# Kernel optimization log

Hardware: AMD Instinct MI355X
Metric: run time of the kernel (lower is better)

Reference implementation:

```python
import jax, jax.numpy as jnp
import numpy as np

# ---- config (mirrors module init_kwargs) ----
PRE_NMS_TOP_N = 4096
POST_NMS_TOP_N = 300
NMS_THRESH = 0.5
MIN_SIZE = 0
IMG_H = 640
IMG_W = 640
BBOX_XFORM_CLIP = float(np.log(1000.0 / 16.0))  # exp clamp in BoxCoder.decode
NEG = -1e9  # score sentinel for suppressed boxes
TO_REMOVE = 1.0


def setup_inputs() -> dict:
    key = jax.random.key(0)
    k1, k2, k3 = jax.random.split(key, 3)
    N, A, H, W, C = 16, 3, 160, 160, 80
    objectness = jax.random.normal(k1, (N, A, H, W), jnp.float32)
    box_regression = jax.random.normal(k2, (N, A * 4, H, W), jnp.float32) * 0.5
    cls = jax.random.normal(k3, (N, A * C, H, W), jnp.float32)
    # grid anchors in xyxy, ordering matches permute_and_flatten (H, W, A)
    stride = IMG_W / W
    xs = (np.arange(W, dtype=np.float32) + 0.5) * stride
    ys = (np.arange(H, dtype=np.float32) + 0.5) * stride
    cy, cx = np.meshgrid(ys, xs, indexing="ij")  # [H,W]
    half = np.array([32.0, 64.0, 128.0], dtype=np.float32) / 2.0  # A anchor sizes
    x1 = cx[..., None] - half
    y1 = cy[..., None] - half
    x2 = cx[..., None] + half - 1.0
    y2 = cy[..., None] + half - 1.0
    anch = np.stack([x1, y1, x2, y2], axis=-1).reshape(-1, 4).astype(np.float32)
    anchors = jnp.broadcast_to(jnp.asarray(anch), (N,) + anch.shape)  # [N, A*H*W, 4]
    return {"anchors": anchors, "objectness": objectness,
            "box_regression": box_regression, "cls": cls}


def _permute_and_flatten(x, N, A, C, H, W):
    # (N, A*C, H, W) -> (N, H*W*A, C)
    return x.reshape(N, A, C, H, W).transpose(0, 3, 4, 1, 2).reshape(N, H * W * A, C)


def _decode(rel, anc):
    # BoxCoder(weights=(1,1,1,1)).decode ; rel, anc: [..., 4] xyxy anchors
    w = anc[..., 2] - anc[..., 0] + TO_REMOVE
    h = anc[..., 3] - anc[..., 1] + TO_REMOVE
    cx = anc[..., 0] + 0.5 * w
    cy = anc[..., 1] + 0.5 * h
    dx, dy = rel[..., 0], rel[..., 1]
    dw = jnp.minimum(rel[..., 2], BBOX_XFORM_CLIP)
    dh = jnp.minimum(rel[..., 3], BBOX_XFORM_CLIP)
    pcx = dx * w + cx
    pcy = dy * h + cy
    pw = jnp.exp(dw) * w
    ph = jnp.exp(dh) * h
    return jnp.stack([pcx - 0.5 * pw, pcy - 0.5 * ph,
                      pcx + 0.5 * pw - 1.0, pcy + 0.5 * ph - 1.0], axis=-1)


def _iou_one_vs_all(b, boxes):
    area_b = (b[2] - b[0] + TO_REMOVE) * (b[3] - b[1] + TO_REMOVE)
    areas = (boxes[:, 2] - boxes[:, 0] + TO_REMOVE) * (boxes[:, 3] - boxes[:, 1] + TO_REMOVE)
    iw = jnp.clip(jnp.minimum(b[2], boxes[:, 2]) - jnp.maximum(b[0], boxes[:, 0]) + TO_REMOVE, 0.0)
    ih = jnp.clip(jnp.minimum(b[3], boxes[:, 3]) - jnp.maximum(b[1], boxes[:, 1]) + TO_REMOVE, 0.0)
    inter = iw * ih
    return inter / (area_b + areas - inter)


def _nms_indices(boxes, scores):
    # greedy NMS, fixed POST_NMS_TOP_N iterations; returns (idx[K], valid[K])
    K = POST_NMS_TOP_N

    def body(i, state):
        sc, idx, val = state
        j = jnp.argmax(sc)
        s = sc[j]
        iou = _iou_one_vs_all(boxes[j], boxes)
        sc = jnp.where(iou > NMS_THRESH, NEG, sc).at[j].set(NEG)
        return sc, idx.at[i].set(j.astype(jnp.int32)), val.at[i].set(s > NEG / 2)

    idx0 = jnp.zeros((K,), jnp.int32)
    val0 = jnp.zeros((K,), bool)
    _, idx, val = jax.lax.fori_loop(0, K, body, (scores, idx0, val0))
    return idx, val


def _forward(anchors, objectness, box_regression, cls):
    N, A, H, W = objectness.shape
    C = cls.shape[1] // A
    obj = jax.nn.sigmoid(_permute_and_flatten(objectness, N, A, 1, H, W).reshape(N, -1))
    cls_f = _permute_and_flatten(cls, N, A, C, H, W)          # [N, P, C]
    reg = _permute_and_flatten(box_regression, N, A, 4, H, W)  # [N, P, 4]

    k1 = min(PRE_NMS_TOP_N, A * H * W)
    scores, topk_idx = jax.lax.top_k(obj, k1)                  # [N, K1]
    b = jnp.arange(N)[:, None]
    reg_t = reg[b, topk_idx]                                   # [N, K1, 4]
    cls_t = cls_f[b, topk_idx]                                 # [N, K1, C]
    anch_t = anchors[b, topk_idx]                              # [N, K1, 4]

    proposals = _decode(reg_t, anch_t)                         # [N, K1, 4]
    labels = jnp.argmax(cls_t, axis=-1) + 1                    # [N, K1]

    # clip_to_image(remove_empty=False)
    x1 = jnp.clip(proposals[..., 0], 0.0, IMG_W - TO_REMOVE)
    y1 = jnp.clip(proposals[..., 1], 0.0, IMG_H - TO_REMOVE)
    x2 = jnp.clip(proposals[..., 2], 0.0, IMG_W - TO_REMOVE)
    y2 = jnp.clip(proposals[..., 3], 0.0, IMG_H - TO_REMOVE)
    boxes = jnp.stack([x1, y1, x2, y2], axis=-1)

    # remove_small_boxes: keep via score masking (keeps shapes static)
    keep = ((x2 - x1 + TO_REMOVE) >= MIN_SIZE) & ((y2 - y1 + TO_REMOVE) >= MIN_SIZE)
    masked_scores = jnp.where(keep, scores, NEG)

    nms_idx, nms_valid = jax.vmap(_nms_indices)(
        jax.lax.stop_gradient(boxes), jax.lax.stop_gradient(masked_scores))

    sel_boxes = boxes[b, nms_idx]                              # [N, K2, 4]
    sel_scores = scores[b, nms_idx]                            # [N, K2]
    sel_labels = labels[b, nms_idx].astype(jnp.float32)

    sel_boxes = jnp.where(nms_valid[..., None], sel_boxes, 0.0)
    sel_scores = jnp.where(nms_valid, sel_scores, 0.0)
    sel_labels = jnp.where(nms_valid, sel_labels, 0.0)
    # [N, K2, 6] = boxes(4) | score(1) | label(1)
    return jnp.concatenate([sel_boxes, sel_scores[..., None], sel_labels[..., None]], axis=-1)


def reference(anchors, objectness, box_regression, cls):
    return _forward(anchors, objectness, box_regression, cls)
```

## Files before the change

kernel.cpp:

```cpp
#include <hip/hip_runtime.h>
#include <math.h>

#define NIMG 16
#define A_ 3
#define H_ 160
#define W_ 160
#define C_ 80
#define HW_ (H_*W_)
#define P_ (HW_*A_)
#define K1 4096
#define K2 300
#define CAND_CAP 8192
#define IMGMAX 639.0f
#define BBOX_CLIP 4.135166556742356f
#define IOU_THR (0.5 + 1.0/67108864.0)

#define RING_ROWS 128
#define GRP 16
#define NGRP (K1/GRP)
#define NTRI 2080
#define TRI_BLOCKS 520

__device__ __forceinline__ unsigned int f2key(float x) {
    unsigned int u = __float_as_uint(x);
    return (u & 0x80000000u) ? ~u : (u | 0x80000000u);
}
__device__ __forceinline__ float key2f(unsigned int k) {
    unsigned int u = (k & 0x80000000u) ? (k & 0x7FFFFFFFu) : ~k;
    return __uint_as_float(u);
}

__global__ __launch_bounds__(256) void k_hist(
        const float* __restrict__ obj, unsigned int* __restrict__ hist) {
    const int n = blockIdx.x / 15;
    const int chunk = blockIdx.x % 15;
    __shared__ unsigned int lh[4096];
    const int tid = threadIdx.x;
    for (int i = tid; i < 4096; i += 256) lh[i] = 0;
    __syncthreads();
    const float* o = obj + (size_t)n * P_ + chunk * 5120;
    for (int q = tid; q < 5120; q += 256) {
        unsigned int k = f2key(o[q]);
        atomicAdd(&lh[k >> 20], 1u);
    }
    __syncthreads();
    for (int i = tid; i < 4096; i += 256) {
        unsigned int v = lh[i];
        if (v) atomicAdd(&hist[n * 4096 + i], v);
    }
}

__global__ __launch_bounds__(64) void k_thresh(
        const unsigned int* __restrict__ hist, unsigned int* __restrict__ Tarr) {
    const int n = blockIdx.x, lane = threadIdx.x;
    const unsigned int* h = hist + n * 4096;
    unsigned int s = 0;
    for (int m = 0; m < 64; ++m) s += h[lane * 64 + m];
    unsigned int t = s;
    for (int off = 1; off < 64; off <<= 1) {
        unsigned int u = __shfl_down(t, off);
        if (lane + off < 64) t += u;
    }
    bool cond = (t >= (unsigned)K1) && (t - s < (unsigned)K1);
    unsigned long long bal = __ballot(cond);
    int cs = __builtin_ctzll(bal);
    unsigned int suf = __shfl(t - s, cs);
    unsigned int h2 = h[cs * 64 + lane];
    unsigned int t2 = h2;
    for (int off = 1; off < 64; off <<= 1) {
        unsigned int u = __shfl_down(t2, off);
        if (lane + off < 64) t2 += u;
    }
    bool cond2 = (suf + t2 >= (unsigned)K1) && (suf + t2 - h2 < (unsigned)K1);
    if (cond2) Tarr[n] = ((unsigned int)(cs * 64 + lane)) << 20;
}

__global__ __launch_bounds__(1024) void k_compact(
        const float* __restrict__ obj, const unsigned int* __restrict__ Tarr,
        unsigned long long* __restrict__ cand, unsigned int* __restrict__ cnt) {
    const int n = blockIdx.x / 75;
    const int q = (blockIdx.x % 75) * 1024 + threadIdx.x;
    const unsigned int T = Tarr[n];
    unsigned int k = f2key(obj[(size_t)n * P_ + q]);
    bool pred = (k >= T);
    const int lane = threadIdx.x & 63, wv = threadIdx.x >> 6;
    unsigned long long m = __ballot(pred);
    __shared__ unsigned int s_wbase[16];
    __shared__ unsigned int s_cnt, s_start;
    if (threadIdx.x == 0) s_cnt = 0;
    __syncthreads();
    if (lane == 0) s_wbase[wv] = atomicAdd(&s_cnt, (unsigned int)__popcll(m));
    __syncthreads();
    if (threadIdx.x == 0) s_start = atomicAdd(&cnt[n], s_cnt);
    __syncthreads();
    if (pred) {
        unsigned int pos = s_start + s_wbase[wv] +
                           (unsigned int)__popcll(m & ((1ull << lane) - 1ull));
        if (pos < CAND_CAP) {
            unsigned int p = (unsigned int)((q % HW_) * A_ + (q / HW_));
            cand[(size_t)n * CAND_CAP + pos] =
                ((unsigned long long)(~k) << 32) | (unsigned long long)p;
        }
    }
}

__global__ __launch_bounds__(1024) void k_sort(
        const unsigned long long* __restrict__ cand,
        const unsigned int* __restrict__ cnt,
        unsigned int* __restrict__ sidx, float* __restrict__ sscore) {
    const int n = blockIdx.x;
    __shared__ unsigned long long S[CAND_CAP];
    const int tid = threadIdx.x;
    const int wv = tid >> 6, lane = tid & 63;
    const int seg = wv * 512;
    unsigned int c = cnt[n]; if (c > CAND_CAP) c = CAND_CAP;
    #pragma unroll
    for (int m = 0; m < 8; ++m) {
        int t = seg + m * 64 + lane;
        S[t] = (t < (int)c) ? cand[(size_t)n * CAND_CAP + t] : 0xFFFFFFFFFFFFFFFFull;
    }
    int prevCross = 1;
    for (int k = 2; k <= CAND_CAP; k <<= 1) {
        for (int j = k >> 1; j > 0; j >>= 1) {
            int cross = (j >= 512);
            if (cross || prevCross) __syncthreads();
            #pragma unroll
            for (int m = 0; m < 8; ++m) {
                int t = seg + m * 64 + lane;
                int ixj = t ^ j;
                if (ixj > t) {
                    unsigned long long a = S[t], b = S[ixj];
                    bool up = ((t & k) == 0);
                    if ((a > b) == up) { S[t] = b; S[ixj] = a; }
                }
            }
            prevCross = cross;
        }
    }
    if (wv < 8) {
        #pragma unroll
        for (int m = 0; m < 8; ++m) {
            int t = seg + m * 64 + lane;
            unsigned long long s = S[t];
            sidx[(size_t)n * K1 + t] = (unsigned int)s;
            float x = key2f(~(unsigned int)(s >> 32));
            sscore[(size_t)n * K1 + t] = 1.0f / (1.0f + expf(-x));
        }
    }
}

__global__ __launch_bounds__(256) void k_decode(
        const unsigned int* __restrict__ sidx, const float* __restrict__ reg,
        float* __restrict__ bx1, float* __restrict__ by1,
        float* __restrict__ bx2, float* __restrict__ by2,
        float* __restrict__ bar) {
#pragma clang fp contract(off)
    const int gid = blockIdx.x * 256 + threadIdx.x;
    const int n = gid >> 12;
    const unsigned int p = sidx[gid];
    const int a  = (int)(p % 3u);
    const int hw = (int)(p / 3u);
    const int hh = hw / W_, ww = hw % W_;

    const float* rb = reg + ((size_t)n * 12 + a * 4) * HW_ + hw;
    float dx = rb[0];
    float dy = rb[HW_];
    float dw = rb[2 * HW_];
    float dh = rb[3 * HW_];

    const int half = 16 << a;
    float a0 = (float)(4 * ww + 2 - half);
    float a1 = (float)(4 * hh + 2 - half);
    float a2 = (float)(4 * ww + 2 + half - 1);
    float a3 = (float)(4 * hh + 2 + half - 1);

    float w  = a2 - a0 + 1.0f;
    float h  = a3 - a1 + 1.0f;
    float cx = a0 + 0.5f * w;
    float cy = a1 + 0.5f * h;
    float dwc = fminf(dw, BBOX_CLIP);
    float dhc = fminf(dh, BBOX_CLIP);
    float pcx = dx * w + cx;
    float pcy = dy * h + cy;
    float pw  = expf(dwc) * w;
    float ph  = expf(dhc) * h;
    float x1 = pcx - 0.5f * pw;
    float y1 = pcy - 0.5f * ph;
    float x2 = pcx + 0.5f * pw - 1.0f;
    float y2 = pcy + 0.5f * ph - 1.0f;
    x1 = fminf(fmaxf(x1, 0.0f), IMGMAX);
    y1 = fminf(fmaxf(y1, 0.0f), IMGMAX);
    x2 = fminf(fmaxf(x2, 0.0f), IMGMAX);
    y2 = fminf(fmaxf(y2, 0.0f), IMGMAX);
    bx1[gid] = x1; by1[gid] = y1; bx2[gid] = x2; by2[gid] = y2;
    bar[gid] = (x2 - x1 + 1.0f) * (y2 - y1 + 1.0f);
}

__global__ __launch_bounds__(256) void k_iou(
        const float* __restrict__ bx1, const float* __restrict__ by1,
        const float* __restrict__ bx2, const float* __restrict__ by2,
        const float* __restrict__ bar,
        unsigned long long* __restrict__ mat) {
#pragma clang fp contract(off)
    const int b = blockIdx.x;
    const int n = b / TRI_BLOCKS;
    const int lane = threadIdx.x & 63, wv = threadIdx.x >> 6;
    const int t = (b % TRI_BLOCKS) * 4 + wv;
    int cw = (int)((sqrtf(8.0f * (float)t + 1.0f) - 1.0f) * 0.5f);
    while (cw * (cw + 1) / 2 > t) --cw;
    while ((cw + 1) * (cw + 2) / 2 <= t) ++cw;
    int R = t - cw * (cw + 1) / 2;
    cw = __builtin_amdgcn_readfirstlane(cw);
    R  = __builtin_amdgcn_readfirstlane(R);

    const size_t nb = (size_t)n * K1;
    const int col = cw * 64 + lane;
    const float cx1 = bx1[nb + col];
    const float cy1 = by1[nb + col];
    const float cx2 = bx2[nb + col];
    const float cy2 = by2[nb + col];
    const float ca  = bar[nb + col];

    const int rbase = R * 64;
    unsigned long long myword = 0ull;
    #pragma unroll 4
    for (int j = 0; j < 64; ++j) {
        const int r = rbase + j;
        const float rx1 = bx1[nb + r];
        const float ry1 = by1[nb + r];
        const float rx2 = bx2[nb + r];
        const float ry2 = by2[nb + r];
        const float ra  = bar[nb + r];
        float iw = fminf(rx2, cx2) - fmaxf(rx1, cx1) + 1.0f;
        float ih = fminf(ry2, cy2) - fmaxf(ry1, cy1) + 1.0f;
        iw = fmaxf(iw, 0.0f);
        ih = fmaxf(ih, 0.0f);
        float inter = iw * ih;
        float denom = (ra + ca) - inter;
        bool pred = (denom > 0.0f) && ((double)inter > (double)denom * IOU_THR);
        unsigned long long balm = __ballot(pred);
        if (lane == j) myword = balm;
    }
    mat[((size_t)n * 64 + cw) * K1 + rbase + lane] = myword;
}

__global__ __launch_bounds__(256) void k_greedy(
        const unsigned long long* __restrict__ mat, int* __restrict__ skept) {
    const int n = blockIdx.x;
    int* kp = skept + n * K2;
    const int tid = threadIdx.x, lane = tid & 63, wv = tid >> 6;
    __shared__ unsigned long long ring[RING_ROWS * 64];
    __shared__ int ctl[2];
    __shared__ int grp[NGRP];
    volatile int* vctl = ctl;
    volatile int* vgrp = grp;
    for (int k = tid; k < K2; k += 256) kp[k] = -1;
    for (int k = tid; k < NGRP; k += 256) grp[k] = 0;
    if (tid == 0) { ctl[0] = 0; ctl[1] = 0; }
    __syncthreads();

    if (wv > 0) {
        const int pw = wv - 1;
        const unsigned long long* Mw = mat + ((size_t)n * 64 + lane) * (size_t)K1;
        for (int g = 0; g < NGRP; ++g) {
            if (((g & 7) % 3) != pw) continue;
            int hint;
            for (;;) {
                if (vctl[1]) return;
                hint = vctl[0];
                if (GRP * g <= hint + (RING_ROWS - GRP)) break;
                __builtin_amdgcn_s_sleep(2);
            }
            if (hint >= GRP * g + GRP) continue;
            const ulonglong2* p = (const ulonglong2*)(Mw + GRP * g);
            ulonglong2 tt[8];
            #pragma unroll
            for (int i = 0; i < 8; ++i) tt[i] = p[i];
            const int base = (GRP * g) & (RING_ROWS - 1);
            #pragma unroll
            for (int i = 0; i < 8; ++i) {
                ring[(base + 2 * i    ) * 64 + lane] = tt[i].x;
                ring[(base + 2 * i + 1) * 64 + lane] = tt[i].y;
            }
            __asm__ __volatile__("s_waitcnt lgkmcnt(0)" ::: "memory");
            if (lane == 0) vgrp[g] = 1;
        }
        return;
    }

    unsigned long long rem = 0ull;
    int cursor = 0;
    for (int it = 0; it < K2; ++it) {
        const int cwrd = cursor >> 6;
        unsigned long long avail = ~rem;
        if (lane < cwrd) avail = 0ull;
        else if (lane == cwrd) avail &= ~((1ull << (cursor & 63)) - 1ull);
        unsigned long long bal = __ballot(avail != 0ull);
        if (bal == 0ull) break;
        const int L = (int)__builtin_ctzll(bal);
        unsigned long long aL = __shfl(avail, L);
        const int c = (L << 6) + (int)__builtin_ctzll(aL);
        if (lane == 0) { kp[it] = c; vctl[0] = c; }
        while (!vgrp[c >> 4]) __builtin_amdgcn_s_sleep(1);
        __asm__ __volatile__("" ::: "memory");
        rem |= ring[(c & (RING_ROWS - 1)) * 64 + lane];
        cursor = c + 1;
    }
    if (lane == 0) vctl[1] = 1;
}

__global__ __launch_bounds__(256) void k_final(
        const int* __restrict__ skept, const unsigned int* __restrict__ sidx,
        const float* __restrict__ sscore, const float* __restrict__ cls,
        const float* __restrict__ bx1, const float* __restrict__ by1,
        const float* __restrict__ bx2, const float* __restrict__ by2,
        float* __restrict__ out) {
    const int g = blockIdx.x * 4 + (threadIdx.x >> 6);
    const int lane = threadIdx.x & 63;
    const int n = g / K2, k = g % K2;
    const int sel = skept[n * K2 + k];
    float* op = out + ((size_t)n * K2 + k) * 6;
    if (sel < 0) {
        if (lane < 6) op[lane] = 0.0f;
        return;
    }
    const unsigned int p = sidx[(size_t)n * K1 + sel];
    const int a  = (int)(p % 3u);
    const int hw = (int)(p / 3u);
    const float* cb = cls + ((size_t)n * 240 + a * 80) * HW_ + hw;
    float v = cb[(size_t)lane * HW_];
    int c = lane;
    if (lane < 16) {
        float v2 = cb[(size_t)(64 + lane) * HW_];
        if (v2 > v) { v = v2; c = 64 + lane; }
    }
    for (int off = 32; off > 0; off >>= 1) {
        float ov = __shfl_down(v, off);
        int   oc = __shfl_down(c, off);
        if ((ov > v) || (ov == v && oc < c)) { v = ov; c = oc; }
    }
    if (lane == 0) {
        op[0] = bx1[(size_t)n * K1 + sel];
        op[1] = by1[(size_t)n * K1 + sel];
        op[2] = bx2[(size_t)n * K1 + sel];
        op[3] = by2[(size_t)n * K1 + sel];
        op[4] = sscore[(size_t)n * K1 + sel];
        op[5] = (float)(c + 1);
    }
}

extern "C" void kernel_launch(void* const* d_in, const int* in_sizes, int n_in,
                              void* d_out, int out_size, void* d_ws, size_t ws_size,
                              hipStream_t stream) {
    (void)in_sizes; (void)n_in; (void)out_size; (void)ws_size;
    const float* objectness = (const float*)d_in[1];
    const float* box_reg    = (const float*)d_in[2];
    const float* cls        = (const float*)d_in[3];
    float* out = (float*)d_out;

    char* ws = (char*)d_ws;
    size_t off = 0;
    unsigned int* hist = (unsigned int*)(ws + off);       off += (size_t)NIMG * 4096 * 4;
    unsigned int* cnt  = (unsigned int*)(ws + off);       off += 64;
    unsigned int* Tarr = (unsigned int*)(ws + off);       off += 64;
    unsigned long long* cand = (unsigned long long*)(ws + off); off += (size_t)NIMG * CAND_CAP * 8;
    unsigned int* sidx = (unsigned int*)(ws + off);       off += (size_t)NIMG * K1 * 4;
    float* sscore = (float*)(ws + off);                   off += (size_t)NIMG * K1 * 4;
    float* bx1 = (float*)(ws + off);                      off += (size_t)NIMG * K1 * 4;
    float* by1 = (float*)(ws + off);                      off += (size_t)NIMG * K1 * 4;
    float* bx2 = (float*)(ws + off);                      off += (size_t)NIMG * K1 * 4;
    float* by2 = (float*)(ws + off);                      off += (size_t)NIMG * K1 * 4;
    float* bar = (float*)(ws + off);                      off += (size_t)NIMG * K1 * 4;
    unsigned long long* mat = (unsigned long long*)(ws + off); off += (size_t)NIMG * K1 * 64 * 8;
    int* skept = (int*)(ws + off);                        off += (size_t)NIMG * K2 * 4;

    hipMemsetAsync(hist, 0, (size_t)NIMG * 4096 * 4 + 64, stream);
    k_hist   <<<240, 256, 0, stream>>>(objectness, hist);
    k_thresh <<<NIMG, 64, 0, stream>>>(hist, Tarr);
    k_compact<<<NIMG * 75, 1024, 0, stream>>>(objectness, Tarr, cand, cnt);
    k_sort   <<<NIMG, 1024, 0, stream>>>(cand, cnt, sidx, sscore);
    k_decode <<<(NIMG * K1) / 256, 256, 0, stream>>>(sidx, box_reg, bx1, by1, bx2, by2, bar);
    k_iou    <<<NIMG * TRI_BLOCKS, 256, 0, stream>>>(bx1, by1, bx2, by2, bar, mat);
    k_greedy <<<NIMG, 256, 0, stream>>>(mat, skept);
    k_final  <<<NIMG * K2 / 4, 256, 0, stream>>>(skept, sidx, sscore, cls,
                                                 bx1, by1, bx2, by2, out);
}
```

Baseline: 773.3 us.

## Split sort across blocks, fuse decode, per-chunk histograms, rework greedy sync

Histograms are written per chunk instead of being merged with global atomics, which removes the memset, and the threshold kernel sums them with 256 threads and also resets the counter. Compaction uses float4 loads with four ballots per thread. The bitonic sort is split into two half-sorts running in parallel blocks plus one merge block, and box decode is fused into the merge kernel. The greedy NMS replaces per-group ready flags with per-producer progress counters, skips loading words that cannot matter, and speculatively reads the ring before waiting. Together these aim to cut launches, serial sort depth and polling overhead, at the cost of more complex synchronisation.

```diff
diff --git a/kernel.cpp b/kernel.cpp
--- a/kernel.cpp
+++ b/kernel.cpp
@@ -20,6 +20,7 @@
 #define NGRP (K1/GRP)
 #define NTRI 2080
 #define TRI_BLOCKS 520
+#define NCHUNK 15
 
 __device__ __forceinline__ unsigned int f2key(float x) {
     unsigned int u = __float_as_uint(x);
@@ -32,168 +33,233 @@
 
 __global__ __launch_bounds__(256) void k_hist(
         const float* __restrict__ obj, unsigned int* __restrict__ hist) {
-    const int n = blockIdx.x / 15;
-    const int chunk = blockIdx.x % 15;
+    const int n = blockIdx.x / NCHUNK;
+    const int chunk = blockIdx.x % NCHUNK;
     __shared__ unsigned int lh[4096];
     const int tid = threadIdx.x;
     for (int i = tid; i < 4096; i += 256) lh[i] = 0;
     __syncthreads();
-    const float* o = obj + (size_t)n * P_ + chunk * 5120;
-    for (int q = tid; q < 5120; q += 256) {
-        unsigned int k = f2key(o[q]);
-        atomicAdd(&lh[k >> 20], 1u);
-    }
-    __syncthreads();
+    const float4* o4 = (const float4*)(obj + (size_t)n * P_ + chunk * 5120);
+    for (int q = tid; q < 1280; q += 256) {
+        float4 v = o4[q];
+        atomicAdd(&lh[f2key(v.x) >> 20], 1u);
+        atomicAdd(&lh[f2key(v.y) >> 20], 1u);
+        atomicAdd(&lh[f2key(v.z) >> 20], 1u);
+        atomicAdd(&lh[f2key(v.w) >> 20], 1u);
+    }
+    __syncthreads();
+    unsigned int* hp = hist + ((size_t)n * NCHUNK + chunk) * 4096;
+    for (int i = tid; i < 4096; i += 256) hp[i] = lh[i];
+}
+
+__global__ __launch_bounds__(256) void k_thresh(
+        const unsigned int* __restrict__ hist, unsigned int* __restrict__ Tarr,
+        unsigned int* __restrict__ cnt) {
+    const int n = blockIdx.x, tid = threadIdx.x;
+    const int lane = tid & 63, wv = tid >> 6;
+    __shared__ unsigned int B[4096];
+    __shared__ unsigned int wtot[4];
     for (int i = tid; i < 4096; i += 256) {
-        unsigned int v = lh[i];
-        if (v) atomicAdd(&hist[n * 4096 + i], v);
-    }
-}
-
-__global__ __launch_bounds__(64) void k_thresh(
-        const unsigned int* __restrict__ hist, unsigned int* __restrict__ Tarr) {
-    const int n = blockIdx.x, lane = threadIdx.x;
-    const unsigned int* h = hist + n * 4096;
-    unsigned int s = 0;
-    for (int m = 0; m < 64; ++m) s += h[lane * 64 + m];
-    unsigned int t = s;
-    for (int off = 1; off < 64; off <<= 1) {
-        unsigned int u = __shfl_down(t, off);
-        if (lane + off < 64) t += u;
-    }
-    bool cond = (t >= (unsigned)K1) && (t - s < (unsigned)K1);
-    unsigned long long bal = __ballot(cond);
-    int cs = __builtin_ctzll(bal);
-    unsigned int suf = __shfl(t - s, cs);
-    unsigned int h2 = h[cs * 64 + lane];
-    unsigned int t2 = h2;
+        unsigned int s = 0;
+        for (int ch = 0; ch < NCHUNK; ++ch)
+            s += hist[((size_t)n * NCHUNK + ch) * 4096 + i];
+        B[i] = s;
+    }
+    __syncthreads();
+    unsigned int ps = 0;
+    #pragma unroll
+    for (int j = 0; j < 16; ++j) ps += B[16 * tid + j];
+    unsigned int t2 = ps;
     for (int off = 1; off < 64; off <<= 1) {
         unsigned int u = __shfl_down(t2, off);
         if (lane + off < 64) t2 += u;
     }
-    bool cond2 = (suf + t2 >= (unsigned)K1) && (suf + t2 - h2 < (unsigned)K1);
-    if (cond2) Tarr[n] = ((unsigned int)(cs * 64 + lane)) << 20;
-}
-
-__global__ __launch_bounds__(1024) void k_compact(
+    if (lane == 0) wtot[wv] = t2;
+    __syncthreads();
+    unsigned int higher = 0;
+    for (int w = wv + 1; w < 4; ++w) higher += wtot[w];
+    const unsigned int cross = higher + t2;
+    const unsigned int above = cross - ps;
+    if (cross >= (unsigned)K1 && above < (unsigned)K1) {
+        unsigned int r = above;
+        for (int j = 15; j >= 0; --j) {
+            r += B[16 * tid + j];
+            if (r >= (unsigned)K1) {
+                Tarr[n] = ((unsigned int)(16 * tid + j)) << 20;
+                break;
+            }
+        }
+    }
+    if (tid == 0) cnt[n] = 0;
+}
+
+__global__ __launch_bounds__(256) void k_compact(
         const float* __restrict__ obj, const unsigned int* __restrict__ Tarr,
         unsigned long long* __restrict__ cand, unsigned int* __restrict__ cnt) {
     const int n = blockIdx.x / 75;
-    const int q = (blockIdx.x % 75) * 1024 + threadIdx.x;
+    const int base = (blockIdx.x % 75) * 1024;
+    const int tid = threadIdx.x, lane = tid & 63, wv = tid >> 6;
     const unsigned int T = Tarr[n];
-    unsigned int k = f2key(obj[(size_t)n * P_ + q]);
-    bool pred = (k >= T);
-    const int lane = threadIdx.x & 63, wv = threadIdx.x >> 6;
-    unsigned long long m = __ballot(pred);
-    __shared__ unsigned int s_wbase[16];
+    float4 v = ((const float4*)(obj + (size_t)n * P_ + base))[tid];
+    unsigned int k0 = f2key(v.x), k1 = f2key(v.y), k2 = f2key(v.z), k3 = f2key(v.w);
+    bool p0 = k0 >= T, p1 = k1 >= T, p2 = k2 >= T, p3 = k3 >= T;
+    unsigned long long m0 = __ballot(p0), m1 = __ballot(p1),
+                       m2 = __ballot(p2), m3 = __ballot(p3);
+    __shared__ unsigned int s_wbase[4];
     __shared__ unsigned int s_cnt, s_start;
-    if (threadIdx.x == 0) s_cnt = 0;
-    __syncthreads();
-    if (lane == 0) s_wbase[wv] = atomicAdd(&s_cnt, (unsigned int)__popcll(m));
-    __syncthreads();
-    if (threadIdx.x == 0) s_start = atomicAdd(&cnt[n], s_cnt);
-    __syncthreads();
-    if (pred) {
-        unsigned int pos = s_start + s_wbase[wv] +
-                           (unsigned int)__popcll(m & ((1ull << lane) - 1ull));
-        if (pos < CAND_CAP) {
-            unsigned int p = (unsigned int)((q % HW_) * A_ + (q / HW_));
-            cand[(size_t)n * CAND_CAP + pos] =
-                ((unsigned long long)(~k) << 32) | (unsigned long long)p;
-        }
-    }
-}
-
-__global__ __launch_bounds__(1024) void k_sort(
+    if (tid == 0) s_cnt = 0;
+    __syncthreads();
+    unsigned int c0 = (unsigned)__popcll(m0), c1 = (unsigned)__popcll(m1),
+                 c2 = (unsigned)__popcll(m2), c3 = (unsigned)__popcll(m3);
+    if (lane == 0) s_wbase[wv] = atomicAdd(&s_cnt, c0 + c1 + c2 + c3);
+    __syncthreads();
+    if (tid == 0) s_start = atomicAdd(&cnt[n], s_cnt);
+    __syncthreads();
+    const unsigned int wb = s_start + s_wbase[wv];
+    const unsigned long long below = (1ull << lane) - 1ull;
+    const int q0 = base + tid * 4;
+    unsigned int pos, q;
+    #define EMIT(pi, ki, oi, qi)                                               \
+        if (pi) {                                                              \
+            pos = wb + (oi); q = (unsigned)(qi);                               \
+            if (pos < CAND_CAP) {                                              \
+                unsigned int p = (q % HW_) * A_ + (q / HW_);                   \
+                cand[(size_t)n * CAND_CAP + pos] =                             \
+                    ((unsigned long long)(~(ki)) << 32) | (unsigned long long)p;\
+            }                                                                  \
+        }
+    EMIT(p0, k0, (unsigned)__popcll(m0 & below), q0 + 0)
+    EMIT(p1, k1, c0 + (unsigned)__popcll(m1 & below), q0 + 1)
+    EMIT(p2, k2, c0 + c1 + (unsigned)__popcll(m2 & below), q0 + 2)
+    EMIT(p3, k3, c0 + c1 + c2 + (unsigned)__popcll(m3 & below), q0 + 3)
+    #undef EMIT
+}
+
+__global__ __launch_bounds__(1024) void k_sort1(
+        const unsigned long long* __restrict__ candIn,
+        const unsigned int* __restrict__ cnt,
+        unsigned long long* __restrict__ candOut) {
+    const int n = blockIdx.x >> 1, half = blockIdx.x & 1;
+    __shared__ unsigned long long S[4096];
+    const int tid = threadIdx.x;
+    const int wv = tid >> 6, lane = tid & 63;
+    const int seg = wv * 256;
+    unsigned int c = cnt[n]; if (c > CAND_CAP) c = CAND_CAP;
+    const int gbase = half * 4096;
+    #pragma unroll
+    for (int m = 0; m < 4; ++m) {
+        int t = seg + m * 64 + lane;
+        int g = gbase + t;
+        S[t] = (g < (int)c) ? candIn[(size_t)n * CAND_CAP + g]
+                            : 0xFFFFFFFFFFFFFFFFull;
+    }
+    int prevCross = 1;
+    for (int k = 2; k <= 4096; k <<= 1) {
+        for (int j = k >> 1; j > 0; j >>= 1) {
+            int cross = (j >= 256);
+            if (cross || prevCross) __syncthreads();
+            #pragma unroll
+            for (int m = 0; m < 4; ++m) {
+                int t = seg + m * 64 + lane;
+                int ixj = t ^ j;
+                if (ixj > t) {
+                    unsigned long long a = S[t], b = S[ixj];
+                    bool up = ((t & k) == 0);
+                    if (half) up = !up;
+                    if ((a > b) == up) { S[t] = b; S[ixj] = a; }
+                }
+            }
+            prevCross = cross;
+        }
+    }
+    __syncthreads();
+    #pragma unroll
+    for (int m = 0; m < 4; ++m) {
+        int t = seg + m * 64 + lane;
+        candOut[(size_t)n * CAND_CAP + gbase + t] = S[t];
+    }
+}
+
+__global__ __launch_bounds__(1024) void k_sort2(
         const unsigned long long* __restrict__ cand,
-        const unsigned int* __restrict__ cnt,
-        unsigned int* __restrict__ sidx, float* __restrict__ sscore) {
+        const float* __restrict__ reg,
+        unsigned int* __restrict__ sidx, float* __restrict__ sscore,
+        float* __restrict__ bx1, float* __restrict__ by1,
+        float* __restrict__ bx2, float* __restrict__ by2,
+        float* __restrict__ bar) {
+#pragma clang fp contract(off)
     const int n = blockIdx.x;
     __shared__ unsigned long long S[CAND_CAP];
     const int tid = threadIdx.x;
     const int wv = tid >> 6, lane = tid & 63;
     const int seg = wv * 512;
-    unsigned int c = cnt[n]; if (c > CAND_CAP) c = CAND_CAP;
     #pragma unroll
     for (int m = 0; m < 8; ++m) {
         int t = seg + m * 64 + lane;
-        S[t] = (t < (int)c) ? cand[(size_t)n * CAND_CAP + t] : 0xFFFFFFFFFFFFFFFFull;
+        S[t] = cand[(size_t)n * CAND_CAP + t];
     }
     int prevCross = 1;
-    for (int k = 2; k <= CAND_CAP; k <<= 1) {
-        for (int j = k >> 1; j > 0; j >>= 1) {
-            int cross = (j >= 512);
-            if (cross || prevCross) __syncthreads();
-            #pragma unroll
-            for (int m = 0; m < 8; ++m) {
-                int t = seg + m * 64 + lane;
-                int ixj = t ^ j;
-                if (ixj > t) {
-                    unsigned long long a = S[t], b = S[ixj];
-                    bool up = ((t & k) == 0);
-                    if ((a > b) == up) { S[t] = b; S[ixj] = a; }
-                }
-            }
-            prevCross = cross;
-        }
-    }
-    if (wv < 8) {
+    for (int j = 4096; j > 0; j >>= 1) {
+        int cross = (j >= 512);
+        if (cross || prevCross) __syncthreads();
         #pragma unroll
         for (int m = 0; m < 8; ++m) {
             int t = seg + m * 64 + lane;
-            unsigned long long s = S[t];
-            sidx[(size_t)n * K1 + t] = (unsigned int)s;
-            float x = key2f(~(unsigned int)(s >> 32));
-            sscore[(size_t)n * K1 + t] = 1.0f / (1.0f + expf(-x));
-        }
-    }
-}
-
-__global__ __launch_bounds__(256) void k_decode(
-        const unsigned int* __restrict__ sidx, const float* __restrict__ reg,
-        float* __restrict__ bx1, float* __restrict__ by1,
-        float* __restrict__ bx2, float* __restrict__ by2,
-        float* __restrict__ bar) {
-#pragma clang fp contract(off)
-    const int gid = blockIdx.x * 256 + threadIdx.x;
-    const int n = gid >> 12;
-    const unsigned int p = sidx[gid];
-    const int a  = (int)(p % 3u);
-    const int hw = (int)(p / 3u);
-    const int hh = hw / W_, ww = hw % W_;
-
-    const float* rb = reg + ((size_t)n * 12 + a * 4) * HW_ + hw;
-    float dx = rb[0];
-    float dy = rb[HW_];
-    float dw = rb[2 * HW_];
-    float dh = rb[3 * HW_];
-
-    const int half = 16 << a;
-    float a0 = (float)(4 * ww + 2 - half);
-    float a1 = (float)(4 * hh + 2 - half);
-    float a2 = (float)(4 * ww + 2 + half - 1);
-    float a3 = (float)(4 * hh + 2 + half - 1);
-
-    float w  = a2 - a0 + 1.0f;
-    float h  = a3 - a1 + 1.0f;
-    float cx = a0 + 0.5f * w;
-    float cy = a1 + 0.5f * h;
-    float dwc = fminf(dw, BBOX_CLIP);
-    float dhc = fminf(dh, BBOX_CLIP);
-    float pcx = dx * w + cx;
-    float pcy = dy * h + cy;
-    float pw  = expf(dwc) * w;
-    float ph  = expf(dhc) * h;
-    float x1 = pcx - 0.5f * pw;
-    float y1 = pcy - 0.5f * ph;
-    float x2 = pcx + 0.5f * pw - 1.0f;
-    float y2 = pcy + 0.5f * ph - 1.0f;
-    x1 = fminf(fmaxf(x1, 0.0f), IMGMAX);
-    y1 = fminf(fmaxf(y1, 0.0f), IMGMAX);
-    x2 = fminf(fmaxf(x2, 0.0f), IMGMAX);
-    y2 = fminf(fmaxf(y2, 0.0f), IMGMAX);
-    bx1[gid] = x1; by1[gid] = y1; bx2[gid] = x2; by2[gid] = y2;
-    bar[gid] = (x2 - x1 + 1.0f) * (y2 - y1 + 1.0f);
+            int ixj = t ^ j;
+            if (ixj > t) {
+                unsigned long long a = S[t], b = S[ixj];
+                if (a > b) { S[t] = b; S[ixj] = a; }
+            }
+        }
+        prevCross = cross;
+    }
+    __syncthreads();
+    #pragma unroll
+    for (int i = 0; i < 4; ++i) {
+        const int t = tid + 1024 * i;
+        const unsigned long long s = S[t];
+        const unsigned int p = (unsigned int)s;
+        const size_t gid = (size_t)n * K1 + t;
+        sidx[gid] = p;
+        float x = key2f(~(unsigned int)(s >> 32));
+        sscore[gid] = 1.0f / (1.0f + expf(-x));
+
+        const int a  = (int)(p % 3u);
+        const int hw = (int)(p / 3u);
+        const int hh = hw / W_, ww = hw % W_;
+        const float* rb = reg + ((size_t)n * 12 + a * 4) * HW_ + hw;
+        float dx = rb[0];
+        float dy = rb[HW_];
+        float dw = rb[2 * HW_];
+        float dh = rb[3 * HW_];
+
+        const int half = 16 << a;
+        float a0 = (float)(4 * ww + 2 - half);
+        float a1 = (float)(4 * hh + 2 - half);
+        float a2 = (float)(4 * ww + 2 + half - 1);
+        float a3 = (float)(4 * hh + 2 + half - 1);
+
+        float w  = a2 - a0 + 1.0f;
+        float h  = a3 - a1 + 1.0f;
+        float cx = a0 + 0.5f * w;
+        float cy = a1 + 0.5f * h;
+        float dwc = fminf(dw, BBOX_CLIP);
+        float dhc = fminf(dh, BBOX_CLIP);
+        float pcx = dx * w + cx;
+        float pcy = dy * h + cy;
+        float pw  = expf(dwc) * w;
+        float ph  = expf(dhc) * h;
+        float x1 = pcx - 0.5f * pw;
+        float y1 = pcy - 0.5f * ph;
+        float x2 = pcx + 0.5f * pw - 1.0f;
+        float y2 = pcy + 0.5f * ph - 1.0f;
+        x1 = fminf(fmaxf(x1, 0.0f), IMGMAX);
+        y1 = fminf(fmaxf(y1, 0.0f), IMGMAX);
+        x2 = fminf(fmaxf(x2, 0.0f), IMGMAX);
+        y2 = fminf(fmaxf(y2, 0.0f), IMGMAX);
+        bx1[gid] = x1; by1[gid] = y1; bx2[gid] = x2; by2[gid] = y2;
+        bar[gid] = (x2 - x1 + 1.0f) * (y2 - y1 + 1.0f);
+    }
 }
 
 __global__ __launch_bounds__(256) void k_iou(
@@ -251,11 +317,11 @@
     const int tid = threadIdx.x, lane = tid & 63, wv = tid >> 6;
     __shared__ unsigned long long ring[RING_ROWS * 64];
     __shared__ int ctl[2];
-    __shared__ int grp[NGRP];
+    __shared__ int prog[3];
     volatile int* vctl = ctl;
-    volatile int* vgrp = grp;
+    volatile int* vprog = prog;
     for (int k = tid; k < K2; k += 256) kp[k] = -1;
-    for (int k = tid; k < NGRP; k += 256) grp[k] = 0;
+    if (tid < 3) prog[tid] = -1;
     if (tid == 0) { ctl[0] = 0; ctl[1] = 0; }
     __syncthreads();
 
@@ -264,32 +330,40 @@
         const unsigned long long* Mw = mat + ((size_t)n * 64 + lane) * (size_t)K1;
         for (int g = 0; g < NGRP; ++g) {
             if (((g & 7) % 3) != pw) continue;
+            if (vctl[1]) return;
             int hint;
             for (;;) {
-                if (vctl[1]) return;
                 hint = vctl[0];
                 if (GRP * g <= hint + (RING_ROWS - GRP)) break;
+                if (vctl[1]) return;
                 __builtin_amdgcn_s_sleep(2);
             }
-            if (hint >= GRP * g + GRP) continue;
-            const ulonglong2* p = (const ulonglong2*)(Mw + GRP * g);
-            ulonglong2 tt[8];
-            #pragma unroll
-            for (int i = 0; i < 8; ++i) tt[i] = p[i];
+            if (hint >= GRP * g + GRP) {
+                if (lane == 0) vprog[pw] = g;
+                continue;
+            }
+            const int wmin = g >> 2;
             const int base = (GRP * g) & (RING_ROWS - 1);
-            #pragma unroll
-            for (int i = 0; i < 8; ++i) {
-                ring[(base + 2 * i    ) * 64 + lane] = tt[i].x;
-                ring[(base + 2 * i + 1) * 64 + lane] = tt[i].y;
+            if (lane >= wmin) {
+                const ulonglong2* p = (const ulonglong2*)(Mw + GRP * g);
+                ulonglong2 tt[8];
+                #pragma unroll
+                for (int i = 0; i < 8; ++i) tt[i] = p[i];
+                #pragma unroll
+                for (int i = 0; i < 8; ++i) {
+                    ring[(base + 2 * i    ) * 64 + lane] = tt[i].x;
+                    ring[(base + 2 * i + 1) * 64 + lane] = tt[i].y;
+                }
             }
             __asm__ __volatile__("s_waitcnt lgkmcnt(0)" ::: "memory");
-            if (lane == 0) vgrp[g] = 1;
+            if (lane == 0) vprog[pw] = g;
         }
         return;
     }
 
     unsigned long long rem = 0ull;
     int cursor = 0;
+    int pc0 = -1, pc1 = -1, pc2 = -1;
     for (int it = 0; it < K2; ++it) {
         const int cwrd = cursor >> 6;
         unsigned long long avail = ~rem;
@@ -301,9 +375,18 @@
         unsigned long long aL = __shfl(avail, L);
         const int c = (L << 6) + (int)__builtin_ctzll(aL);
         if (lane == 0) { kp[it] = c; vctl[0] = c; }
-        while (!vgrp[c >> 4]) __builtin_amdgcn_s_sleep(1);
-        __asm__ __volatile__("" ::: "memory");
-        rem |= ring[(c & (RING_ROWS - 1)) * 64 + lane];
+        const int g = c >> 4;
+        const int owner = (g & 7) % 3;
+        unsigned long long r1 = ring[(c & (RING_ROWS - 1)) * 64 + lane];
+        int pcv = (owner == 0) ? pc0 : ((owner == 1) ? pc1 : pc2);
+        if (pcv < g) {
+            int pv;
+            while ((pv = vprog[owner]) < g) __builtin_amdgcn_s_sleep(1);
+            if (owner == 0) pc0 = pv; else if (owner == 1) pc1 = pv; else pc2 = pv;
+            __asm__ __volatile__("" ::: "memory");
+            r1 = ring[(c & (RING_ROWS - 1)) * 64 + lane];
+        }
+        rem |= r1;
         cursor = c + 1;
     }
     if (lane == 0) vctl[1] = 1;
@@ -360,7 +443,7 @@
 
     char* ws = (char*)d_ws;
     size_t off = 0;
-    unsigned int* hist = (unsigned int*)(ws + off);       off += (size_t)NIMG * 4096 * 4;
+    unsigned int* hist = (unsigned int*)(ws + off);       off += (size_t)NIMG * NCHUNK * 4096 * 4;
     unsigned int* cnt  = (unsigned int*)(ws + off);       off += 64;
     unsigned int* Tarr = (unsigned int*)(ws + off);       off += 64;
     unsigned long long* cand = (unsigned long long*)(ws + off); off += (size_t)NIMG * CAND_CAP * 8;
@@ -374,12 +457,12 @@
     unsigned long long* mat = (unsigned long long*)(ws + off); off += (size_t)NIMG * K1 * 64 * 8;
     int* skept = (int*)(ws + off);                        off += (size_t)NIMG * K2 * 4;
 
-    hipMemsetAsync(hist, 0, (size_t)NIMG * 4096 * 4 + 64, stream);
-    k_hist   <<<240, 256, 0, stream>>>(objectness, hist);
-    k_thresh <<<NIMG, 64, 0, stream>>>(hist, Tarr);
-    k_compact<<<NIMG * 75, 1024, 0, stream>>>(objectness, Tarr, cand, cnt);
-    k_sort   <<<NIMG, 1024, 0, stream>>>(cand, cnt, sidx, sscore);
-    k_decode <<<(NIMG * K1) / 256, 256, 0, stream>>>(sidx, box_reg, bx1, by1, bx2, by2, bar);
+    k_hist   <<<NIMG * NCHUNK, 256, 0, stream>>>(objectness, hist);
+    k_thresh <<<NIMG, 256, 0, stream>>>(hist, Tarr, cnt);
+    k_compact<<<NIMG * 75, 256, 0, stream>>>(objectness, Tarr, cand, cnt);
+    k_sort1  <<<NIMG * 2, 1024, 0, stream>>>(cand, cnt, cand);
+    k_sort2  <<<NIMG, 1024, 0, stream>>>(cand, box_reg, sidx, sscore,
+                                         bx1, by1, bx2, by2, bar);
     k_iou    <<<NIMG * TRI_BLOCKS, 256, 0, stream>>>(bx1, by1, bx2, by2, bar, mat);
     k_greedy <<<NIMG, 256, 0, stream>>>(mat, skept);
     k_final  <<<NIMG * K2 / 4, 256, 0, stream>>>(skept, sidx, sscore, cls,
```

Result: no change. 761.4 us (-1.5%).
